# Kernel optimization log

Hardware: AMD Instinct MI355X
Metric: run time of the kernel (lower is better)

Reference implementation:

```python
import jax, jax.numpy as jnp
import numpy as np

N_NODES = 100000
N_EDGES = 1600000
IN_CH = 64
HID_CH = 64
NUM_LAYERS = 3


def _init_linear(key, out_ch, in_ch, bias=True):
    # torch nn.Linear default init: U(-1/sqrt(in), 1/sqrt(in))
    bound = 1.0 / np.sqrt(in_ch)
    kw, kb = jax.random.split(key)
    W = jax.random.uniform(kw, (out_ch, in_ch), jnp.float32, -bound, bound)
    if bias:
        b = jax.random.uniform(kb, (out_ch,), jnp.float32, -bound, bound)
        return W, b
    return W, None


def setup_inputs() -> dict:
    key = jax.random.key(0)
    ks = jax.random.split(key, 8)
    x = jax.random.normal(ks[0], (N_NODES, IN_CH), jnp.float32)
    edge_index = jax.random.randint(ks[1], (2, N_EDGES), 0, N_NODES, jnp.int64)
    inp = {"x": x, "edge_index": edge_index}
    in_dims = [IN_CH] + [HID_CH] * (NUM_LAYERS - 1)
    for i, d_in in enumerate(in_dims):
        kl, kr = jax.random.split(ks[2 + i])
        Wl, bl = _init_linear(kl, HID_CH, d_in, bias=True)   # lin_l: aggregated neighbors (has bias)
        Wr, _ = _init_linear(kr, HID_CH, d_in, bias=False)   # lin_r: root/self features (no bias)
        inp[f"Wl{i}"] = Wl
        inp[f"bl{i}"] = bl
        inp[f"Wr{i}"] = Wr
    return inp


def _sage_conv(x, src, dst, deg_inv, Wl, bl, Wr):
    # mean aggregation of source features into destination nodes
    msg = x[src]                                              # [E, d]  (irregular gather)
    agg = jax.ops.segment_sum(msg, dst, num_segments=N_NODES)  # [N, d] (irregular scatter)
    agg = agg * deg_inv[:, None]
    return agg @ Wl.T + bl + x @ Wr.T


def reference(x, edge_index, Wl0, bl0, Wr0, Wl1, bl1, Wr1, Wl2, bl2, Wr2):
    src, dst = edge_index[0], edge_index[1]
    deg = jax.ops.segment_sum(jnp.ones((N_EDGES,), x.dtype), dst, num_segments=N_NODES)
    deg_inv = 1.0 / jnp.maximum(deg, 1.0)
    params = [(Wl0, bl0, Wr0), (Wl1, bl1, Wr1), (Wl2, bl2, Wr2)]
    h = x
    for i, (Wl, bl, Wr) in enumerate(params):
        h = _sage_conv(h, src, dst, deg_inv, Wl, bl, Wr)
        if i < NUM_LAYERS - 1:
            h = jax.nn.relu(h)  # dropout is identity in eval mode
    return h
```

## Files before the change

kernel.cpp:

```cpp
#include <hip/hip_runtime.h>
#include <hip/hip_bf16.h>

#define N_NODES 100000
#define N_EDGES 1600000
#define CH 64
#define NRANGE 8
#define CAP (N_EDGES / 4)
#define LCAP 384
#define CHUNK 2048


__device__ __forceinline__ unsigned short f2bf(float f) {
    unsigned int u = __float_as_uint(f);
    u += 0x7FFF + ((u >> 16) & 1);
    return (unsigned short)(u >> 16);
}
__device__ __forceinline__ float bf2f(unsigned short b) {
    return __uint_as_float(((unsigned int)b) << 16);
}


__global__ __launch_bounds__(256) void k_bin(const int* __restrict__ src,
                                             const int* __restrict__ dst,
                                             int* __restrict__ bcur,
                                             int* __restrict__ bsrc,
                                             int* __restrict__ bdst,
                                             int E, int span) {
    __shared__ int lcnt[NRANGE];
    __shared__ int lbase[NRANGE];
    __shared__ int lbd[NRANGE][LCAP];
    __shared__ int lbs[NRANGE][LCAP];
    int tid = threadIdx.x;

    for (int base = blockIdx.x * CHUNK; base < E; base += gridDim.x * CHUNK) {
        if (tid < NRANGE) lcnt[tid] = 0;
        __syncthreads();

#pragma unroll
        for (int k = 0; k < CHUNK / 256; ++k) {
            int i = base + k * 256 + tid;
            if (i < E) {
                int d = dst[i];
                int s = src[i];
                int r = d / span;
                int pos = atomicAdd(&lcnt[r], 1);
                if (pos < LCAP) {
                    lbd[r][pos] = d;
                    lbs[r][pos] = s;
                } else {
                    int gi = atomicAdd(&bcur[r], 1);
                    if (gi < CAP) { bdst[r * CAP + gi] = d; bsrc[r * CAP + gi] = s; }
                }
            }
        }
        __syncthreads();

        if (tid < NRANGE) {
            int c = lcnt[tid]; if (c > LCAP) c = LCAP;
            lcnt[tid]  = c;
            lbase[tid] = atomicAdd(&bcur[tid], c);
        }
        __syncthreads();

#pragma unroll
        for (int r = 0; r < NRANGE; ++r) {
            int c = lcnt[r];
            int b = lbase[r];
            for (int i = tid; i < c; i += 256) {
                int gi = b + i;
                if (gi < CAP) {
                    bdst[r * CAP + gi] = lbd[r][i];
                    bsrc[r * CAP + gi] = lbs[r][i];
                }
            }
        }
        __syncthreads();
    }
}

__global__ __launch_bounds__(256) void k_count(const int* __restrict__ bcur,
                                               const int* __restrict__ bdst,
                                               int* __restrict__ cnt) {
    int r    = blockIdx.x & (NRANGE - 1);
    int gtid = (blockIdx.x >> 3) * blockDim.x + threadIdx.x;
    int gnth = (gridDim.x >> 3) * blockDim.x;
    int n = bcur[r]; if (n > CAP) n = CAP;
    const int* bp = bdst + r * CAP;
    for (int i = gtid; i < n; i += gnth) atomicAdd(&cnt[bp[i]], 1);
}

__global__ __launch_bounds__(1024) void k_scanA(const int* __restrict__ cnt, int N,
                                                int* __restrict__ rowp, int* __restrict__ bsum) {
    __shared__ int s[1024];
    int t = threadIdx.x;
    int g = blockIdx.x * 1024 + t;
    int v = (g < N) ? cnt[g] : 0;
    s[t] = v;
    __syncthreads();
    for (int off = 1; off < 1024; off <<= 1) {
        int x = (t >= off) ? s[t - off] : 0;
        __syncthreads();
        s[t] += x;
        __syncthreads();
    }
    if (g < N) rowp[g] = s[t] - v;
    if (t == 1023) bsum[blockIdx.x] = s[1023];
}

__global__ __launch_bounds__(1024) void k_scanB(int* __restrict__ bsum, int nb) {
    __shared__ int s[1024];
    int t = threadIdx.x;
    int v = (t < nb) ? bsum[t] : 0;
    s[t] = v;
    __syncthreads();
    for (int off = 1; off < 1024; off <<= 1) {
        int x = (t >= off) ? s[t - off] : 0;
        __syncthreads();
        s[t] += x;
        __syncthreads();
    }
    if (t < nb) bsum[t] = s[t] - v;
}

__global__ void k_scanC(int* __restrict__ rowp, const int* __restrict__ cnt,
                        const int* __restrict__ bsum, int* __restrict__ cursor,
                        float* __restrict__ dinv, int N) {
    int g = blockIdx.x * blockDim.x + threadIdx.x;
    if (g < N) {
        int r = rowp[g] + bsum[g >> 10];
        rowp[g]   = r;
        cursor[g] = r;
        int d = cnt[g];
        dinv[g] = 1.0f / (float)(d > 1 ? d : 1);
    }
}

__global__ __launch_bounds__(256) void k_fill2(const int* __restrict__ bcur,
                                               const int* __restrict__ bsrc,
                                               const int* __restrict__ bdst,
                                               int* __restrict__ cursor,
                                               int* __restrict__ col) {
    int r    = blockIdx.x & (NRANGE - 1);
    int gtid = (blockIdx.x >> 3) * blockDim.x + threadIdx.x;
    int gnth = (gridDim.x >> 3) * blockDim.x;
    int n = bcur[r]; if (n > CAP) n = CAP;
    const int* bd = bdst + r * CAP;
    const int* bs = bsrc + r * CAP;
    for (int i = gtid; i < n; i += gnth) {
        int d = bd[i];
        int s = bs[i];
        col[atomicAdd(&cursor[d], 1)] = s;
    }
}

__global__ __launch_bounds__(256) void k_transform(const float* __restrict__ h,
                                                   const float* __restrict__ Wl,
                                                   const float* __restrict__ bl,
                                                   const float* __restrict__ Wr,
                                                   unsigned short* __restrict__ T,
                                                   float* __restrict__ S, int N) {
    int lane = threadIdx.x & 63;
    float wl[CH], wr[CH];
    const float4* Wl4 = (const float4*)(Wl + lane * CH);
    const float4* Wr4 = (const float4*)(Wr + lane * CH);
#pragma unroll
    for (int q = 0; q < CH / 4; ++q) {
        float4 a = Wl4[q];
        wl[4 * q] = a.x; wl[4 * q + 1] = a.y; wl[4 * q + 2] = a.z; wl[4 * q + 3] = a.w;
        float4 b = Wr4[q];
        wr[4 * q] = b.x; wr[4 * q + 1] = b.y; wr[4 * q + 2] = b.z; wr[4 * q + 3] = b.w;
    }
    float bias = bl[lane];

    int wid    = (blockIdx.x * blockDim.x + threadIdx.x) >> 6;
    int nwaves = (gridDim.x * blockDim.x) >> 6;
    for (int n = wid; n < N; n += nwaves) {
        float hv = h[n * CH + lane];
        float ol = 0.f, orr = 0.f;
#pragma unroll
        for (int c = 0; c < CH; ++c) {
            float hc = __uint_as_float(__builtin_amdgcn_readlane(__float_as_uint(hv), c));
            ol  += hc * wl[c];
            orr += hc * wr[c];
        }
        T[n * CH + lane] = f2bf(ol);
        S[n * CH + lane] = orr + bias;
    }
}

__global__ __launch_bounds__(256) void k_gather(const unsigned short* __restrict__ T,
                                                const float* __restrict__ S,
                                                const int* __restrict__ rowp,
                                                const int* __restrict__ cnt,
                                                const float* __restrict__ dinv,
                                                const int* __restrict__ col,
                                                float* __restrict__ out,
                                                int relu, int N) {
    int li = threadIdx.x & 31;
    int n  = blockIdx.x * 8 + (threadIdx.x >> 5);
    if (n >= N) return;

    int start = rowp[n];
    int deg   = cnt[n];
    const int* cp = col + start;

    float a0 = 0.f, a1 = 0.f, b0 = 0.f, b1 = 0.f;
    float c0 = 0.f, c1 = 0.f, d0 = 0.f, d1 = 0.f;
    int e = 0;
    for (; e + 8 <= deg; e += 8) {
        int s0 = cp[e + 0];
        int s1 = cp[e + 1];
        int s2 = cp[e + 2];
        int s3 = cp[e + 3];
        int s4 = cp[e + 4];
        int s5 = cp[e + 5];
        int s6 = cp[e + 6];
        int s7 = cp[e + 7];
        unsigned u0 = *(const unsigned*)(T + (size_t)s0 * CH + 2 * li);
        unsigned u1 = *(const unsigned*)(T + (size_t)s1 * CH + 2 * li);
        unsigned u2 = *(const unsigned*)(T + (size_t)s2 * CH + 2 * li);
        unsigned u3 = *(const unsigned*)(T + (size_t)s3 * CH + 2 * li);
        unsigned u4 = *(const unsigned*)(T + (size_t)s4 * CH + 2 * li);
        unsigned u5 = *(const unsigned*)(T + (size_t)s5 * CH + 2 * li);
        unsigned u6 = *(const unsigned*)(T + (size_t)s6 * CH + 2 * li);
        unsigned u7 = *(const unsigned*)(T + (size_t)s7 * CH + 2 * li);
        a0 += bf2f((unsigned short)u0); a1 += bf2f((unsigned short)(u0 >> 16));
        b0 += bf2f((unsigned short)u1); b1 += bf2f((unsigned short)(u1 >> 16));
        c0 += bf2f((unsigned short)u2); c1 += bf2f((unsigned short)(u2 >> 16));
        d0 += bf2f((unsigned short)u3); d1 += bf2f((unsigned short)(u3 >> 16));
        a0 += bf2f((unsigned short)u4); a1 += bf2f((unsigned short)(u4 >> 16));
        b0 += bf2f((unsigned short)u5); b1 += bf2f((unsigned short)(u5 >> 16));
        c0 += bf2f((unsigned short)u6); c1 += bf2f((unsigned short)(u6 >> 16));
        d0 += bf2f((unsigned short)u7); d1 += bf2f((unsigned short)(u7 >> 16));
    }
    for (; e < deg; ++e) {
        int s = cp[e];
        unsigned u = *(const unsigned*)(T + (size_t)s * CH + 2 * li);
        a0 += bf2f((unsigned short)u); a1 += bf2f((unsigned short)(u >> 16));
    }
    float r0 = (a0 + b0) + (c0 + d0);
    float r1 = (a1 + b1) + (c1 + d1);

    float dv = dinv[n];
    float2 sv = *(const float2*)(S + (size_t)n * CH + 2 * li);
    float o0 = sv.x + r0 * dv;
    float o1 = sv.y + r1 * dv;
    if (relu) { o0 = fmaxf(o0, 0.f); o1 = fmaxf(o1, 0.f); }
    *(float2*)(out + (size_t)n * CH + 2 * li) = make_float2(o0, o1);
}


extern "C" void kernel_launch(void* const* d_in, const int* in_sizes, int n_in,
                              void* d_out, int out_size, void* d_ws, size_t ws_size,
                              hipStream_t stream) {
    const float* x   = (const float*)d_in[0];
    const int*   ei  = (const int*)d_in[1];
    const int E = in_sizes[1] / 2;
    const int N = in_sizes[0] / CH;
    const int* src = ei;
    const int* dst = ei + E;

    const float* Wl[3] = { (const float*)d_in[2], (const float*)d_in[5], (const float*)d_in[8] };
    const float* bl[3] = { (const float*)d_in[3], (const float*)d_in[6], (const float*)d_in[9] };
    const float* Wr[3] = { (const float*)d_in[4], (const float*)d_in[7], (const float*)d_in[10] };

    char* ws = (char*)d_ws;
    size_t off = 0;
    auto take = [&](size_t bytes) { char* p = ws + off; off += (bytes + 255) & ~(size_t)255; return p; };
    int*            cnt    = (int*)           take((size_t)N * 4);
    int*            rowp   = (int*)           take((size_t)(N + 1) * 4);
    int*            cursor = (int*)           take((size_t)N * 4);
    float*          dinv   = (float*)         take((size_t)N * 4);
    int*            bsum   = (int*)           take(4096);
    int*            bcur   = (int*)           take(256);
    int*            col    = (int*)           take((size_t)E * 4);
    int*            bsrc   = (int*)           take((size_t)NRANGE * CAP * 4);
    int*            bdst   = (int*)           take((size_t)NRANGE * CAP * 4);
    unsigned short* T      = (unsigned short*)take((size_t)N * CH * 2);
    float*          S      = (float*)         take((size_t)N * CH * 4);
    float*          buf0   = (float*)         take((size_t)N * CH * 4);
    float*          outp   = (float*)d_out;

    hipMemsetAsync(cnt, 0, (size_t)N * 4, stream);
    hipMemsetAsync(bcur, 0, 256, stream);

    int tb = 256;
    int span = (N + NRANGE - 1) / NRANGE;
    k_bin<<<(N_EDGES + CHUNK - 1) / CHUNK, tb, 0, stream>>>(src, dst, bcur, bsrc, bdst, E, span);
    k_count<<<1024, tb, 0, stream>>>(bcur, bdst, cnt);

    int nb = (N + 1023) / 1024;
    k_scanA<<<nb, 1024, 0, stream>>>(cnt, N, rowp, bsum);
    k_scanB<<<1, 1024, 0, stream>>>(bsum, nb);
    k_scanC<<<(N + tb - 1) / tb, tb, 0, stream>>>(rowp, cnt, bsum, cursor, dinv, N);
    k_fill2<<<1024, tb, 0, stream>>>(bcur, bsrc, bdst, cursor, col);

    int gblocks = (N + 7) / 8;
    k_transform<<<1024, 256, 0, stream>>>(x, Wl[0], bl[0], Wr[0], T, S, N);
    k_gather<<<gblocks, 256, 0, stream>>>(T, S, rowp, cnt, dinv, col, buf0, 1, N);
    k_transform<<<1024, 256, 0, stream>>>(buf0, Wl[1], bl[1], Wr[1], T, S, N);
    k_gather<<<gblocks, 256, 0, stream>>>(T, S, rowp, cnt, dinv, col, buf0, 1, N);
    k_transform<<<1024, 256, 0, stream>>>(buf0, Wl[2], bl[2], Wr[2], T, S, N);
    k_gather<<<gblocks, 256, 0, stream>>>(T, S, rowp, cnt, dinv, col, outp, 0, N);
}
```

Measured before the change: 554.5 us.

## Build CSR columns per node sub-range in LDS instead of global atomics

```diff
diff --git a/kernel.cpp b/kernel.cpp
--- a/kernel.cpp
+++ b/kernel.cpp
@@ -8,6 +8,9 @@
 #define CAP (N_EDGES / 4)
 #define LCAP 384
 #define CHUNK 2048
+#define BPR 16
+#define SLOTS 14336
+#define SSPAN_MAX 800
 
 
 __device__ __forceinline__ unsigned short f2bf(float f) {
@@ -123,34 +126,60 @@
 }
 
 __global__ void k_scanC(int* __restrict__ rowp, const int* __restrict__ cnt,
-                        const int* __restrict__ bsum, int* __restrict__ cursor,
+                        const int* __restrict__ bsum,
                         float* __restrict__ dinv, int N) {
     int g = blockIdx.x * blockDim.x + threadIdx.x;
     if (g < N) {
         int r = rowp[g] + bsum[g >> 10];
-        rowp[g]   = r;
-        cursor[g] = r;
+        rowp[g] = r;
         int d = cnt[g];
         dinv[g] = 1.0f / (float)(d > 1 ? d : 1);
-    }
-}
-
-__global__ __launch_bounds__(256) void k_fill2(const int* __restrict__ bcur,
+        if (g == N - 1) rowp[N] = r + d;
+    }
+}
+
+__global__ __launch_bounds__(256) void k_fill3(const int* __restrict__ bcur,
                                                const int* __restrict__ bsrc,
                                                const int* __restrict__ bdst,
-                                               int* __restrict__ cursor,
-                                               int* __restrict__ col) {
-    int r    = blockIdx.x & (NRANGE - 1);
-    int gtid = (blockIdx.x >> 3) * blockDim.x + threadIdx.x;
-    int gnth = (gridDim.x >> 3) * blockDim.x;
+                                               const int* __restrict__ rowp,
+                                               int* __restrict__ col, int N) {
+    __shared__ int scol[SLOTS];
+    __shared__ int rlds[SSPAN_MAX];
+    __shared__ int lcur[SSPAN_MAX];
+    int r = blockIdx.x & (NRANGE - 1);
+    int b = blockIdx.x >> 3;
+    int span  = (N + NRANGE - 1) / NRANGE;
+    int rlo   = r * span;
+    int rhi   = min(rlo + span, N);
+    int sspan = (span + BPR - 1) / BPR;
+    int nlo   = rlo + b * sspan;
+    int nhi   = min(nlo + sspan, rhi);
+    if (nlo >= nhi) return;
+    int tid = threadIdx.x;
+    int nn  = nhi - nlo;
+
+    for (int i = tid; i < nn; i += 256) { rlds[i] = rowp[nlo + i]; lcur[i] = 0; }
+    __syncthreads();
+    int base  = rlds[0];
+    int total = rowp[nhi] - base;
+
     int n = bcur[r]; if (n > CAP) n = CAP;
     const int* bd = bdst + r * CAP;
     const int* bs = bsrc + r * CAP;
-    for (int i = gtid; i < n; i += gnth) {
+    for (int i = tid; i < n; i += 256) {
         int d = bd[i];
-        int s = bs[i];
-        col[atomicAdd(&cursor[d], 1)] = s;
-    }
+        if (d >= nlo && d < nhi) {
+            int li  = d - nlo;
+            int pos = rlds[li] - base + atomicAdd(&lcur[li], 1);
+            int s   = bs[i];
+            if (pos < SLOTS) scol[pos] = s;
+            else             col[base + pos] = s;
+        }
+    }
+    __syncthreads();
+
+    int m = total < SLOTS ? total : SLOTS;
+    for (int i = tid; i < m; i += 256) col[base + i] = scol[i];
 }
 
 __global__ __launch_bounds__(256) void k_transform(const float* __restrict__ h,
@@ -269,7 +298,6 @@
     auto take = [&](size_t bytes) { char* p = ws + off; off += (bytes + 255) & ~(size_t)255; return p; };
     int*            cnt    = (int*)           take((size_t)N * 4);
     int*            rowp   = (int*)           take((size_t)(N + 1) * 4);
-    int*            cursor = (int*)           take((size_t)N * 4);
     float*          dinv   = (float*)         take((size_t)N * 4);
     int*            bsum   = (int*)           take(4096);
     int*            bcur   = (int*)           take(256);
@@ -292,8 +320,8 @@
     int nb = (N + 1023) / 1024;
     k_scanA<<<nb, 1024, 0, stream>>>(cnt, N, rowp, bsum);
     k_scanB<<<1, 1024, 0, stream>>>(bsum, nb);
-    k_scanC<<<(N + tb - 1) / tb, tb, 0, stream>>>(rowp, cnt, bsum, cursor, dinv, N);
-    k_fill2<<<1024, tb, 0, stream>>>(bcur, bsrc, bdst, cursor, col);
+    k_scanC<<<(N + tb - 1) / tb, tb, 0, stream>>>(rowp, cnt, bsum, dinv, N);
+    k_fill3<<<NRANGE * BPR, tb, 0, stream>>>(bcur, bsrc, bdst, rowp, col, N);
 
     int gblocks = (N + 7) / 8;
     k_transform<<<1024, 256, 0, stream>>>(x, Wl[0], bl[0], Wr[0], T, S, N);
```

After: 767.0 us. 38.3% more time.
